# Performance work log

Hardware: AMD Instinct MI355X
Metric: run time of the kernel (lower is better)

Reference implementation:

```python
import jax, jax.numpy as jnp
import numpy as np

N, E = 50000, 800000
DIN, DH, DOUT = 128, 128, 64


def setup_inputs() -> dict:
    key = jax.random.key(0)
    ks = jax.random.split(key, 18)
    s = 0.05
    inp = {
        "x": jax.random.normal(ks[0], (N, DIN), dtype=jnp.float32),
        "edge_index": jax.random.randint(ks[1], (2, E), 0, N, dtype=jnp.int64),
        # conv1 MLP: Linear(DIN,DH), Linear(DH,DH)
        "c1_w1": jax.random.normal(ks[2], (DIN, DH), dtype=jnp.float32) * s,
        "c1_b1": jax.random.normal(ks[3], (DH,), dtype=jnp.float32) * s,
        "c1_w2": jax.random.normal(ks[4], (DH, DH), dtype=jnp.float32) * s,
        "c1_b2": jax.random.normal(ks[5], (DH,), dtype=jnp.float32) * s,
        # conv2 MLP
        "c2_w1": jax.random.normal(ks[6], (DH, DH), dtype=jnp.float32) * s,
        "c2_b1": jax.random.normal(ks[7], (DH,), dtype=jnp.float32) * s,
        "c2_w2": jax.random.normal(ks[8], (DH, DH), dtype=jnp.float32) * s,
        "c2_b2": jax.random.normal(ks[9], (DH,), dtype=jnp.float32) * s,
        # conv3 MLP
        "c3_w1": jax.random.normal(ks[10], (DH, DH), dtype=jnp.float32) * s,
        "c3_b1": jax.random.normal(ks[11], (DH,), dtype=jnp.float32) * s,
        "c3_w2": jax.random.normal(ks[12], (DH, DH), dtype=jnp.float32) * s,
        "c3_b2": jax.random.normal(ks[13], (DH,), dtype=jnp.float32) * s,
        # output head
        "lin1_w": jax.random.normal(ks[14], (DH, DH), dtype=jnp.float32) * s,
        "lin1_b": jax.random.normal(ks[15], (DH,), dtype=jnp.float32) * s,
        "lin2_w": jax.random.normal(ks[16], (DH, DOUT), dtype=jnp.float32) * s,
        "lin2_b": jax.random.normal(ks[17], (DOUT,), dtype=jnp.float32) * s,
    }
    return inp


def _gin_conv(h, src, dst, w1, b1, w2, b2):
    # PyG GINConv, eps=0: MLP((1+eps)*x + sum_{j->i} x_j)
    agg = jax.ops.segment_sum(h[src], dst, num_segments=h.shape[0])  # [N, D]
    z = h + agg
    z = jax.nn.relu(z @ w1 + b1)
    return jax.nn.relu(z @ w2 + b2)


def reference(x, edge_index, c1_w1, c1_b1, c1_w2, c1_b2,
              c2_w1, c2_b1, c2_w2, c2_b2,
              c3_w1, c3_b1, c3_w2, c3_b2,
              lin1_w, lin1_b, lin2_w, lin2_b):
    src, dst = edge_index[0], edge_index[1]
    h = _gin_conv(x, src, dst, c1_w1, c1_b1, c1_w2, c1_b2)
    h = jax.nn.relu(h)  # redundant after MLP ReLU, but faithful to source
    h = _gin_conv(h, src, dst, c2_w1, c2_b1, c2_w2, c2_b2)
    h = jax.nn.relu(h)
    h = _gin_conv(h, src, dst, c3_w1, c3_b1, c3_w2, c3_b2)
    h = jax.nn.relu(h @ lin1_w + lin1_b)
    return h @ lin2_w + lin2_b  # [N, DOUT]
```

## Files before the change

kernel.cpp:

```cpp
#include <hip/hip_runtime.h>
#include <hip/hip_bf16.h>

typedef __attribute__((ext_vector_type(8))) short bf16x8;
typedef __attribute__((ext_vector_type(4))) float f32x4;

#define DH 128
#define DOUT 64

static __device__ __forceinline__ unsigned short f2bf(float f) {
    __hip_bfloat16 h = __float2bfloat16(f);
    return *(unsigned short*)&h;
}
static __device__ __forceinline__ void acc2(float& a0, float& a1, unsigned int u) {
    a0 += __uint_as_float(u << 16);
    a1 += __uint_as_float(u & 0xffff0000u);
}


struct WPrep {
    const float* src[8];
    unsigned short* dst[8];
};

__global__ void prep_kernel(const float* __restrict__ x, unsigned short* __restrict__ xb,
                            unsigned short* __restrict__ hA, unsigned short* __restrict__ hB,
                            int n4, WPrep p, int* __restrict__ cnt,
                            int* __restrict__ esrc, int Epad, int N_) {
    int id = blockIdx.x * blockDim.x + threadIdx.x;
    if (id < n4) {
        float4 v = ((const float4*)x)[id];
        ushort4 b;
        b.x = f2bf(v.x); b.y = f2bf(v.y); b.z = f2bf(v.z); b.w = f2bf(v.w);
        ((ushort4*)xb)[id] = b;
        return;
    }
    id -= n4;
    if (id < N_) { cnt[id] = 0; return; }
    id -= N_;
    if (id < 7 * 16384 + 8192) {
        int m, off;
        if (id < 7 * 16384) { m = id >> 14; off = id & 16383; }
        else { m = 7; off = id - 7 * 16384; }
        int shift = (m == 7) ? 6 : 7;
        int nc = 1 << shift;
        int k = off >> shift;
        int n = off & (nc - 1);
        p.dst[m][n * 128 + k] = f2bf(p.src[m][off]);
        return;
    }
    id -= 7 * 16384 + 8192;
    if (id < 3 * 128) {
        int j = id & 127, w = id >> 7;
        if (w == 0) xb[(size_t)N_ * 128 + j] = 0;
        else if (w == 1) hA[(size_t)N_ * 128 + j] = 0;
        else hB[(size_t)N_ * 128 + j] = 0;
        return;
    }
    id -= 384;
    if (id < Epad) esrc[id] = N_ << 8;
}


__global__ void hist_kernel(const int* __restrict__ dst, int* __restrict__ cnt,
                            int* __restrict__ rank, int E, int n) {
    int e = blockIdx.x * blockDim.x + threadIdx.x;
    if (e < E) {
        int d = dst[e];
        if ((unsigned)d < (unsigned)n) rank[e] = atomicAdd(&cnt[d], 1);
    }
}

__global__ void scan1_kernel(const int* __restrict__ cnt, int* __restrict__ rp_part,
                             int* __restrict__ bsum, int n) {
    __shared__ int s[256];
    int tid = threadIdx.x;
    int i = blockIdx.x * 256 + tid;
    int v = (i < n) ? ((cnt[i] + 7) & ~7) : 0;
    s[tid] = v;
    __syncthreads();
    for (int off = 1; off < 256; off <<= 1) {
        int t = (tid >= off) ? s[tid - off] : 0;
        __syncthreads();
        s[tid] += t;
        __syncthreads();
    }
    if (i <= n) rp_part[i] = s[tid] - v;
    if (tid == 255) bsum[blockIdx.x] = s[255];
}

__global__ void scan2_kernel(int* __restrict__ bsum, int nb) {
    __shared__ int s[256];
    int tid = threadIdx.x;
    int v = (tid < nb) ? bsum[tid] : 0;
    s[tid] = v;
    __syncthreads();
    for (int off = 1; off < 256; off <<= 1) {
        int t = (tid >= off) ? s[tid - off] : 0;
        __syncthreads();
        s[tid] += t;
        __syncthreads();
    }
    if (tid < nb) bsum[tid] = s[tid] - v;
}

__global__ void scan3_fill_kernel(const int* __restrict__ rp_part, const int* __restrict__ bsum,
                                  int* __restrict__ row_ptr,
                                  const int* __restrict__ src, const int* __restrict__ dst,
                                  const int* __restrict__ rank, int* __restrict__ esrc,
                                  int n, int E) {
    int gid = blockIdx.x * blockDim.x + threadIdx.x;
    if (gid <= n) row_ptr[gid] = rp_part[gid] + bsum[gid >> 8];
    if (gid < E) {
        int d = dst[gid];
        if ((unsigned)d < (unsigned)n)
            esrc[rp_part[d] + bsum[d >> 8] + rank[gid]] = src[gid] << 8;
    }
}


template <bool HEAD>
__launch_bounds__(256, 8)
__global__ void layer_kernel(const unsigned short* __restrict__ h,
                             const int* __restrict__ rp,
                             const int* __restrict__ esrc,
                             const unsigned short* __restrict__ W1t,
                             const float* __restrict__ b1,
                             const unsigned short* __restrict__ W2t,
                             const float* __restrict__ b2,
                             const unsigned short* __restrict__ W3t,
                             const float* __restrict__ b3,
                             const unsigned short* __restrict__ W4t,
                             const float* __restrict__ b4,
                             void* __restrict__ outp, int M) {
    constexpr int LDA = 128 + 8;
    __shared__ __align__(16) unsigned short As[16][LDA];
    __shared__ __align__(16) unsigned short Zs[16][LDA];

    int tid = threadIdx.x;
    int wave = __builtin_amdgcn_readfirstlane(tid >> 6);
    int lane = tid & 63;
    int row0 = blockIdx.x * 16;
    int nd0 = row0 + wave * 4;

    const char* hc = (const char*)h;
    unsigned voff = (unsigned)lane << 2;

#pragma unroll
    for (int i = 0; i < 4; ++i) {
        int nd = nd0 + i;
        int rb = __builtin_amdgcn_readfirstlane(rp[nd]);
        int re = __builtin_amdgcn_readfirstlane(rp[nd + 1]);
        unsigned su = *(const unsigned*)(hc + ((size_t)(unsigned)nd << 8) + voff);
        float a0 = 0.f, a1 = 0.f;
        for (int r = rb; r < re; r += 8) {
            int o0 = __builtin_amdgcn_readfirstlane(esrc[r + 0]);
            int o1 = __builtin_amdgcn_readfirstlane(esrc[r + 1]);
            int o2 = __builtin_amdgcn_readfirstlane(esrc[r + 2]);
            int o3 = __builtin_amdgcn_readfirstlane(esrc[r + 3]);
            int o4 = __builtin_amdgcn_readfirstlane(esrc[r + 4]);
            int o5 = __builtin_amdgcn_readfirstlane(esrc[r + 5]);
            int o6 = __builtin_amdgcn_readfirstlane(esrc[r + 6]);
            int o7 = __builtin_amdgcn_readfirstlane(esrc[r + 7]);
            unsigned u0 = *(const unsigned*)(hc + o0 + voff);
            unsigned u1 = *(const unsigned*)(hc + o1 + voff);
            unsigned u2 = *(const unsigned*)(hc + o2 + voff);
            unsigned u3 = *(const unsigned*)(hc + o3 + voff);
            unsigned u4 = *(const unsigned*)(hc + o4 + voff);
            unsigned u5 = *(const unsigned*)(hc + o5 + voff);
            unsigned u6 = *(const unsigned*)(hc + o6 + voff);
            unsigned u7 = *(const unsigned*)(hc + o7 + voff);
            acc2(a0, a1, u0);
            acc2(a0, a1, u1);
            acc2(a0, a1, u2);
            acc2(a0, a1, u3);
            acc2(a0, a1, u4);
            acc2(a0, a1, u5);
            acc2(a0, a1, u6);
            acc2(a0, a1, u7);
        }
        acc2(a0, a1, su);
        unsigned pv = (unsigned)f2bf(a0) | ((unsigned)f2bf(a1) << 16);
        *(unsigned*)&As[wave * 4 + i][lane * 2] = pv;
    }
    __syncthreads();

    int quad = lane >> 4;
    int l16 = lane & 15;

    bf16x8 af[4];
#pragma unroll
    for (int kt = 0; kt < 4; ++kt)
        af[kt] = *(const bf16x8*)(&As[l16][kt * 32 + quad * 8]);
#pragma unroll
    for (int p = 0; p < 2; ++p) {
        int ncol = (wave * 2 + p) * 16 + l16;
        const unsigned short* wp = W1t + ncol * 128 + quad * 8;
        f32x4 a = {0.f, 0.f, 0.f, 0.f};
#pragma unroll
        for (int kt = 0; kt < 4; ++kt)
            a = __builtin_amdgcn_mfma_f32_16x16x32_bf16(
                af[kt], *(const bf16x8*)(wp + kt * 32), a, 0, 0, 0);
        float bs = b1[ncol];
#pragma unroll
        for (int r = 0; r < 4; ++r) {
            float v = a[r] + bs;
            if (v < 0.f) v = 0.f;
            Zs[quad * 4 + r][ncol] = f2bf(v);
        }
    }
    __syncthreads();

    bf16x8 zf[4];
#pragma unroll
    for (int kt = 0; kt < 4; ++kt)
        zf[kt] = *(const bf16x8*)(&Zs[l16][kt * 32 + quad * 8]);
#pragma unroll
    for (int p = 0; p < 2; ++p) {
        int ncol = (wave * 2 + p) * 16 + l16;
        const unsigned short* wp = W2t + ncol * 128 + quad * 8;
        f32x4 a = {0.f, 0.f, 0.f, 0.f};
#pragma unroll
        for (int kt = 0; kt < 4; ++kt)
            a = __builtin_amdgcn_mfma_f32_16x16x32_bf16(
                zf[kt], *(const bf16x8*)(wp + kt * 32), a, 0, 0, 0);
        float bs = b2[ncol];
#pragma unroll
        for (int r = 0; r < 4; ++r) {
            float v = a[r] + bs;
            if (v < 0.f) v = 0.f;
            if (HEAD) {
                As[quad * 4 + r][ncol] = f2bf(v);
            } else {
                int grow = row0 + quad * 4 + r;
                if (grow < M)
                    ((unsigned short*)outp)[(size_t)grow * 128 + ncol] = f2bf(v);
            }
        }
    }

    if (HEAD) {
        __syncthreads();
        bf16x8 hf[4];
#pragma unroll
        for (int kt = 0; kt < 4; ++kt)
            hf[kt] = *(const bf16x8*)(&As[l16][kt * 32 + quad * 8]);
#pragma unroll
        for (int p = 0; p < 2; ++p) {
            int ncol = (wave * 2 + p) * 16 + l16;
            const unsigned short* wp = W3t + ncol * 128 + quad * 8;
            f32x4 a = {0.f, 0.f, 0.f, 0.f};
#pragma unroll
            for (int kt = 0; kt < 4; ++kt)
                a = __builtin_amdgcn_mfma_f32_16x16x32_bf16(
                    hf[kt], *(const bf16x8*)(wp + kt * 32), a, 0, 0, 0);
            float bs = b3[ncol];
#pragma unroll
            for (int r = 0; r < 4; ++r) {
                float v = a[r] + bs;
                if (v < 0.f) v = 0.f;
                Zs[quad * 4 + r][ncol] = f2bf(v);
            }
        }
        __syncthreads();
        bf16x8 gf[4];
#pragma unroll
        for (int kt = 0; kt < 4; ++kt)
            gf[kt] = *(const bf16x8*)(&Zs[l16][kt * 32 + quad * 8]);
        {
            int ncol = wave * 16 + l16;
            const unsigned short* wp = W4t + ncol * 128 + quad * 8;
            f32x4 a = {0.f, 0.f, 0.f, 0.f};
#pragma unroll
            for (int kt = 0; kt < 4; ++kt)
                a = __builtin_amdgcn_mfma_f32_16x16x32_bf16(
                    gf[kt], *(const bf16x8*)(wp + kt * 32), a, 0, 0, 0);
            float bs = b4[ncol];
#pragma unroll
            for (int r = 0; r < 4; ++r) {
                int grow = row0 + quad * 4 + r;
                if (grow < M)
                    ((float*)outp)[(size_t)grow * 64 + ncol] = a[r] + bs;
            }
        }
    }
}


extern "C" void kernel_launch(void* const* d_in, const int* in_sizes, int n_in,
                              void* d_out, int out_size, void* d_ws, size_t ws_size,
                              hipStream_t stream) {
    const float* x = (const float*)d_in[0];
    const int* ei = (const int*)d_in[1];
    int N = in_sizes[0] / DH;
    int E = in_sizes[1] / 2;
    const int* src = ei;
    const int* dstv = ei + E;
    int Epad = E + 7 * N + 1024;

    char* ws = (char*)d_ws;
    size_t off = 0;
    auto alloc = [&](size_t bytes) -> void* {
        void* p = ws + off;
        off += (bytes + 255) & ~(size_t)255;
        return p;
    };
    unsigned short* xb = (unsigned short*)alloc((size_t)(N + 1) * DH * 2);
    unsigned short* hA = (unsigned short*)alloc((size_t)(N + 1) * DH * 2);
    unsigned short* hB = (unsigned short*)alloc((size_t)(N + 1) * DH * 2);
    unsigned short* wt[8];
    for (int m = 0; m < 8; ++m) wt[m] = (unsigned short*)alloc(16384 * 2);
    int* cnt     = (int*)alloc((size_t)N * 4);
    int* rp_part = (int*)alloc((size_t)(N + 1) * 4);
    int* row_ptr = (int*)alloc((size_t)(N + 1) * 4);
    int* rank    = (int*)alloc((size_t)E * 4);
    int* bsum    = (int*)alloc(256 * 4);
    int* esrc    = (int*)alloc((size_t)Epad * 4);

    WPrep wp;
    wp.src[0] = (const float*)d_in[2];
    wp.src[1] = (const float*)d_in[4];
    wp.src[2] = (const float*)d_in[6];
    wp.src[3] = (const float*)d_in[8];
    wp.src[4] = (const float*)d_in[10];
    wp.src[5] = (const float*)d_in[12];
    wp.src[6] = (const float*)d_in[14];
    wp.src[7] = (const float*)d_in[16];
    for (int m = 0; m < 8; ++m) wp.dst[m] = wt[m];
    int n4 = N * DH / 4;
    int prep_items = n4 + N + 7 * 16384 + 8192 + 384 + Epad;
    prep_kernel<<<(prep_items + 255) / 256, 256, 0, stream>>>(
        x, xb, hA, hB, n4, wp, cnt, esrc, Epad, N);

    int nb = (N + 1 + 255) / 256;
    int eb = (E + 255) / 256;
    hist_kernel<<<eb, 256, 0, stream>>>(dstv, cnt, rank, E, N);
    scan1_kernel<<<nb, 256, 0, stream>>>(cnt, rp_part, bsum, N);
    scan2_kernel<<<1, 256, 0, stream>>>(bsum, nb);
    scan3_fill_kernel<<<eb, 256, 0, stream>>>(rp_part, bsum, row_ptr,
                                              src, dstv, rank, esrc, N, E);

    int gb = (N + 15) / 16;

    const float* c1b1 = (const float*)d_in[3];
    const float* c1b2 = (const float*)d_in[5];
    const float* c2b1 = (const float*)d_in[7];
    const float* c2b2 = (const float*)d_in[9];
    const float* c3b1 = (const float*)d_in[11];
    const float* c3b2 = (const float*)d_in[13];
    const float* l1b  = (const float*)d_in[15];
    const float* l2b  = (const float*)d_in[17];

    layer_kernel<false><<<gb, 256, 0, stream>>>(
        xb, row_ptr, esrc, wt[0], c1b1, wt[1], c1b2,
        nullptr, nullptr, nullptr, nullptr, hA, N);
    layer_kernel<false><<<gb, 256, 0, stream>>>(
        hA, row_ptr, esrc, wt[2], c2b1, wt[3], c2b2,
        nullptr, nullptr, nullptr, nullptr, hB, N);
    layer_kernel<true><<<gb, 256, 0, stream>>>(
        hB, row_ptr, esrc, wt[4], c3b1, wt[5], c3b2,
        wt[6], l1b, wt[7], l2b, d_out, N);
}
```

Baseline: 323.7 us.

## Stage block edge indices in LDS and software-pipeline the neighbor gather

```diff
diff --git a/kernel.cpp b/kernel.cpp
--- a/kernel.cpp
+++ b/kernel.cpp
@@ -119,7 +119,7 @@
 
 
 template <bool HEAD>
-__launch_bounds__(256, 8)
+__launch_bounds__(256, 6)
 __global__ void layer_kernel(const unsigned short* __restrict__ h,
                              const int* __restrict__ rp,
                              const int* __restrict__ esrc,
@@ -133,8 +133,10 @@
                              const float* __restrict__ b4,
                              void* __restrict__ outp, int M) {
     constexpr int LDA = 128 + 8;
+    constexpr int CAP = 2048;
     __shared__ __align__(16) unsigned short As[16][LDA];
     __shared__ __align__(16) unsigned short Zs[16][LDA];
+    __shared__ int sIdx[CAP];
 
     int tid = threadIdx.x;
     int wave = __builtin_amdgcn_readfirstlane(tid >> 6);
@@ -145,41 +147,62 @@
     const char* hc = (const char*)h;
     unsigned voff = (unsigned)lane << 2;
 
+    int wb = rp[row0];
+    int C = rp[min(row0 + 16, M)] - wb;
+
+    int b[4], e[4];
+    unsigned su[4];
+    float a0[4] = {0.f, 0.f, 0.f, 0.f}, a1[4] = {0.f, 0.f, 0.f, 0.f};
 #pragma unroll
     for (int i = 0; i < 4; ++i) {
         int nd = nd0 + i;
-        int rb = __builtin_amdgcn_readfirstlane(rp[nd]);
-        int re = __builtin_amdgcn_readfirstlane(rp[nd + 1]);
-        unsigned su = *(const unsigned*)(hc + ((size_t)(unsigned)nd << 8) + voff);
-        float a0 = 0.f, a1 = 0.f;
-        for (int r = rb; r < re; r += 8) {
-            int o0 = __builtin_amdgcn_readfirstlane(esrc[r + 0]);
-            int o1 = __builtin_amdgcn_readfirstlane(esrc[r + 1]);
-            int o2 = __builtin_amdgcn_readfirstlane(esrc[r + 2]);
-            int o3 = __builtin_amdgcn_readfirstlane(esrc[r + 3]);
-            int o4 = __builtin_amdgcn_readfirstlane(esrc[r + 4]);
-            int o5 = __builtin_amdgcn_readfirstlane(esrc[r + 5]);
-            int o6 = __builtin_amdgcn_readfirstlane(esrc[r + 6]);
-            int o7 = __builtin_amdgcn_readfirstlane(esrc[r + 7]);
-            unsigned u0 = *(const unsigned*)(hc + o0 + voff);
-            unsigned u1 = *(const unsigned*)(hc + o1 + voff);
-            unsigned u2 = *(const unsigned*)(hc + o2 + voff);
-            unsigned u3 = *(const unsigned*)(hc + o3 + voff);
-            unsigned u4 = *(const unsigned*)(hc + o4 + voff);
-            unsigned u5 = *(const unsigned*)(hc + o5 + voff);
-            unsigned u6 = *(const unsigned*)(hc + o6 + voff);
-            unsigned u7 = *(const unsigned*)(hc + o7 + voff);
-            acc2(a0, a1, u0);
-            acc2(a0, a1, u1);
-            acc2(a0, a1, u2);
-            acc2(a0, a1, u3);
-            acc2(a0, a1, u4);
-            acc2(a0, a1, u5);
-            acc2(a0, a1, u6);
-            acc2(a0, a1, u7);
-        }
-        acc2(a0, a1, su);
-        unsigned pv = (unsigned)f2bf(a0) | ((unsigned)f2bf(a1) << 16);
+        int ndc = min(nd, M);
+        int nd1 = min(nd + 1, M);
+        b[i] = rp[ndc] - wb;
+        e[i] = rp[nd1] - wb;
+        su[i] = *(const unsigned*)(hc + ((size_t)(unsigned)ndc << 8) + voff);
+    }
+
+    for (int p0 = 0; p0 < C; p0 += CAP) {
+        int cend = min(C, p0 + CAP);
+        for (int i = tid; i < cend - p0; i += 256) sIdx[i] = esrc[wb + p0 + i];
+        __syncthreads();
+#pragma unroll
+        for (int i = 0; i < 4; ++i) {
+            int nb = max(b[i], p0) - p0;
+            int ne = min(e[i], cend) - p0;
+            if (nb < ne) {
+                int idxA[8];
+                unsigned uA[8];
+#pragma unroll
+                for (int t = 0; t < 8; ++t) idxA[t] = sIdx[nb + t];
+#pragma unroll
+                for (int t = 0; t < 8; ++t)
+                    uA[t] = *(const unsigned*)(hc + (unsigned)idxA[t] + voff);
+                for (int r = nb + 8; r < ne; r += 8) {
+                    int idxB[8];
+                    unsigned uB[8];
+#pragma unroll
+                    for (int t = 0; t < 8; ++t) idxB[t] = sIdx[r + t];
+#pragma unroll
+                    for (int t = 0; t < 8; ++t)
+                        uB[t] = *(const unsigned*)(hc + (unsigned)idxB[t] + voff);
+#pragma unroll
+                    for (int t = 0; t < 8; ++t) acc2(a0[i], a1[i], uA[t]);
+#pragma unroll
+                    for (int t = 0; t < 8; ++t) { uA[t] = uB[t]; }
+                }
+#pragma unroll
+                for (int t = 0; t < 8; ++t) acc2(a0[i], a1[i], uA[t]);
+            }
+        }
+        __syncthreads();
+    }
+
+#pragma unroll
+    for (int i = 0; i < 4; ++i) {
+        acc2(a0[i], a1[i], su[i]);
+        unsigned pv = (unsigned)f2bf(a0[i]) | ((unsigned)f2bf(a1[i]) << 16);
         *(unsigned*)&As[wave * 4 + i][lane * 2] = pv;
     }
     __syncthreads();
```

Result: no change. 321.5 us (-0.7%).

## Drop CSR padding to multiples of 8 and fuse preprocessing launches

Applied to the files above, without the earlier changes.

```diff
diff --git a/kernel.cpp b/kernel.cpp
--- a/kernel.cpp
+++ b/kernel.cpp
@@ -22,10 +22,11 @@
     unsigned short* dst[8];
 };
 
-__global__ void prep_kernel(const float* __restrict__ x, unsigned short* __restrict__ xb,
-                            unsigned short* __restrict__ hA, unsigned short* __restrict__ hB,
-                            int n4, WPrep p, int* __restrict__ cnt,
-                            int* __restrict__ esrc, int Epad, int N_) {
+__global__ void prep_hist_kernel(const float* __restrict__ x, unsigned short* __restrict__ xb,
+                                 unsigned short* __restrict__ hA, unsigned short* __restrict__ hB,
+                                 int n4, WPrep p,
+                                 const int* __restrict__ dstv, int* __restrict__ cnt,
+                                 int* __restrict__ rank, int E, int N_) {
     int id = blockIdx.x * blockDim.x + threadIdx.x;
     if (id < n4) {
         float4 v = ((const float4*)x)[id];
@@ -35,8 +36,6 @@
         return;
     }
     id -= n4;
-    if (id < N_) { cnt[id] = 0; return; }
-    id -= N_;
     if (id < 7 * 16384 + 8192) {
         int m, off;
         if (id < 7 * 16384) { m = id >> 14; off = id & 16383; }
@@ -57,25 +56,19 @@
         return;
     }
     id -= 384;
-    if (id < Epad) esrc[id] = N_ << 8;
-}
-
-
-__global__ void hist_kernel(const int* __restrict__ dst, int* __restrict__ cnt,
-                            int* __restrict__ rank, int E, int n) {
-    int e = blockIdx.x * blockDim.x + threadIdx.x;
-    if (e < E) {
-        int d = dst[e];
-        if ((unsigned)d < (unsigned)n) rank[e] = atomicAdd(&cnt[d], 1);
-    }
-}
+    if (id < E) {
+        int d = dstv[id];
+        if ((unsigned)d < (unsigned)N_) rank[id] = atomicAdd(&cnt[d], 1);
+    }
+}
+
 
 __global__ void scan1_kernel(const int* __restrict__ cnt, int* __restrict__ rp_part,
                              int* __restrict__ bsum, int n) {
     __shared__ int s[256];
     int tid = threadIdx.x;
     int i = blockIdx.x * 256 + tid;
-    int v = (i < n) ? ((cnt[i] + 7) & ~7) : 0;
+    int v = (i < n) ? cnt[i] : 0;
     s[tid] = v;
     __syncthreads();
     for (int off = 1; off < 256; off <<= 1) {
@@ -88,32 +81,34 @@
     if (tid == 255) bsum[blockIdx.x] = s[255];
 }
 
-__global__ void scan2_kernel(int* __restrict__ bsum, int nb) {
-    __shared__ int s[256];
-    int tid = threadIdx.x;
-    int v = (tid < nb) ? bsum[tid] : 0;
-    s[tid] = v;
-    __syncthreads();
-    for (int off = 1; off < 256; off <<= 1) {
-        int t = (tid >= off) ? s[tid - off] : 0;
-        __syncthreads();
-        s[tid] += t;
-        __syncthreads();
-    }
-    if (tid < nb) bsum[tid] = s[tid] - v;
-}
-
 __global__ void scan3_fill_kernel(const int* __restrict__ rp_part, const int* __restrict__ bsum,
                                   int* __restrict__ row_ptr,
                                   const int* __restrict__ src, const int* __restrict__ dst,
                                   const int* __restrict__ rank, int* __restrict__ esrc,
-                                  int n, int E) {
-    int gid = blockIdx.x * blockDim.x + threadIdx.x;
-    if (gid <= n) row_ptr[gid] = rp_part[gid] + bsum[gid >> 8];
+                                  int n, int E, int nb) {
+    __shared__ int sb[256];
+    int tid = threadIdx.x;
+    {
+        int v = (tid < nb) ? bsum[tid] : 0;
+        sb[tid] = v;
+        __syncthreads();
+        for (int off = 1; off < 256; off <<= 1) {
+            int t = (tid >= off) ? sb[tid - off] : 0;
+            __syncthreads();
+            sb[tid] += t;
+            __syncthreads();
+        }
+        int incl = sb[tid];
+        __syncthreads();
+        sb[tid] = incl - v;
+        __syncthreads();
+    }
+    int gid = blockIdx.x * 256 + tid;
+    if (gid <= n) row_ptr[gid] = rp_part[gid] + sb[gid >> 8];
     if (gid < E) {
         int d = dst[gid];
         if ((unsigned)d < (unsigned)n)
-            esrc[rp_part[d] + bsum[d >> 8] + rank[gid]] = src[gid] << 8;
+            esrc[rp_part[d] + sb[d >> 8] + rank[gid]] = src[gid] << 8;
     }
 }
 
@@ -147,28 +142,28 @@
 
 #pragma unroll
     for (int i = 0; i < 4; ++i) {
-        int nd = nd0 + i;
-        int rb = __builtin_amdgcn_readfirstlane(rp[nd]);
-        int re = __builtin_amdgcn_readfirstlane(rp[nd + 1]);
+        int nd = min(nd0 + i, M - 1);
+        int rb = rp[nd], re = rp[nd + 1];
         unsigned su = *(const unsigned*)(hc + ((size_t)(unsigned)nd << 8) + voff);
         float a0 = 0.f, a1 = 0.f;
-        for (int r = rb; r < re; r += 8) {
-            int o0 = __builtin_amdgcn_readfirstlane(esrc[r + 0]);
-            int o1 = __builtin_amdgcn_readfirstlane(esrc[r + 1]);
-            int o2 = __builtin_amdgcn_readfirstlane(esrc[r + 2]);
-            int o3 = __builtin_amdgcn_readfirstlane(esrc[r + 3]);
-            int o4 = __builtin_amdgcn_readfirstlane(esrc[r + 4]);
-            int o5 = __builtin_amdgcn_readfirstlane(esrc[r + 5]);
-            int o6 = __builtin_amdgcn_readfirstlane(esrc[r + 6]);
-            int o7 = __builtin_amdgcn_readfirstlane(esrc[r + 7]);
-            unsigned u0 = *(const unsigned*)(hc + o0 + voff);
-            unsigned u1 = *(const unsigned*)(hc + o1 + voff);
-            unsigned u2 = *(const unsigned*)(hc + o2 + voff);
-            unsigned u3 = *(const unsigned*)(hc + o3 + voff);
-            unsigned u4 = *(const unsigned*)(hc + o4 + voff);
-            unsigned u5 = *(const unsigned*)(hc + o5 + voff);
-            unsigned u6 = *(const unsigned*)(hc + o6 + voff);
-            unsigned u7 = *(const unsigned*)(hc + o7 + voff);
+        int j = rb;
+        for (; j + 8 <= re; j += 8) {
+            int o0 = esrc[j + 0];
+            int o1 = esrc[j + 1];
+            int o2 = esrc[j + 2];
+            int o3 = esrc[j + 3];
+            int o4 = esrc[j + 4];
+            int o5 = esrc[j + 5];
+            int o6 = esrc[j + 6];
+            int o7 = esrc[j + 7];
+            unsigned u0 = *(const unsigned*)(hc + (unsigned)o0 + voff);
+            unsigned u1 = *(const unsigned*)(hc + (unsigned)o1 + voff);
+            unsigned u2 = *(const unsigned*)(hc + (unsigned)o2 + voff);
+            unsigned u3 = *(const unsigned*)(hc + (unsigned)o3 + voff);
+            unsigned u4 = *(const unsigned*)(hc + (unsigned)o4 + voff);
+            unsigned u5 = *(const unsigned*)(hc + (unsigned)o5 + voff);
+            unsigned u6 = *(const unsigned*)(hc + (unsigned)o6 + voff);
+            unsigned u7 = *(const unsigned*)(hc + (unsigned)o7 + voff);
             acc2(a0, a1, u0);
             acc2(a0, a1, u1);
             acc2(a0, a1, u2);
@@ -177,6 +172,18 @@
             acc2(a0, a1, u5);
             acc2(a0, a1, u6);
             acc2(a0, a1, u7);
+        }
+        for (; j + 2 <= re; j += 2) {
+            int o0 = esrc[j], o1 = esrc[j + 1];
+            unsigned u0 = *(const unsigned*)(hc + (unsigned)o0 + voff);
+            unsigned u1 = *(const unsigned*)(hc + (unsigned)o1 + voff);
+            acc2(a0, a1, u0);
+            acc2(a0, a1, u1);
+        }
+        for (; j < re; ++j) {
+            int o0 = esrc[j];
+            unsigned u0 = *(const unsigned*)(hc + (unsigned)o0 + voff);
+            acc2(a0, a1, u0);
         }
         acc2(a0, a1, su);
         unsigned pv = (unsigned)f2bf(a0) | ((unsigned)f2bf(a1) << 16);
@@ -295,7 +302,6 @@
     int E = in_sizes[1] / 2;
     const int* src = ei;
     const int* dstv = ei + E;
-    int Epad = E + 7 * N + 1024;
 
     char* ws = (char*)d_ws;
     size_t off = 0;
@@ -314,7 +320,7 @@
     int* row_ptr = (int*)alloc((size_t)(N + 1) * 4);
     int* rank    = (int*)alloc((size_t)E * 4);
     int* bsum    = (int*)alloc(256 * 4);
-    int* esrc    = (int*)alloc((size_t)Epad * 4);
+    int* esrc    = (int*)alloc((size_t)E * 4);
 
     WPrep wp;
     wp.src[0] = (const float*)d_in[2];
@@ -326,18 +332,21 @@
     wp.src[6] = (const float*)d_in[14];
     wp.src[7] = (const float*)d_in[16];
     for (int m = 0; m < 8; ++m) wp.dst[m] = wt[m];
+
+    hipMemsetAsync(cnt, 0, (size_t)N * 4, stream);
+
     int n4 = N * DH / 4;
-    int prep_items = n4 + N + 7 * 16384 + 8192 + 384 + Epad;
-    prep_kernel<<<(prep_items + 255) / 256, 256, 0, stream>>>(
-        x, xb, hA, hB, n4, wp, cnt, esrc, Epad, N);
-
-    int nb = (N + 1 + 255) / 256;
+    int prep_items = n4 + 7 * 16384 + 8192 + 384 + E;
+    prep_hist_kernel<<<(prep_items + 255) / 256, 256, 0, stream>>>(
+        x, xb, hA, hB, n4, wp, dstv, cnt, rank, E, N);
+
+    int nb = (N + 255) / 256;
+    int nb1 = (N + 1 + 255) / 256;
     int eb = (E + 255) / 256;
-    hist_kernel<<<eb, 256, 0, stream>>>(dstv, cnt, rank, E, N);
-    scan1_kernel<<<nb, 256, 0, stream>>>(cnt, rp_part, bsum, N);
-    scan2_kernel<<<1, 256, 0, stream>>>(bsum, nb);
-    scan3_fill_kernel<<<eb, 256, 0, stream>>>(rp_part, bsum, row_ptr,
-                                              src, dstv, rank, esrc, N, E);
+    scan1_kernel<<<nb1, 256, 0, stream>>>(cnt, rp_part, bsum, N);
+    int s3blocks = eb > nb1 ? eb : nb1;
+    scan3_fill_kernel<<<s3blocks, 256, 0, stream>>>(rp_part, bsum, row_ptr,
+                                                    src, dstv, rank, esrc, N, E, nb);
 
     int gb = (N + 15) / 16;
 
```

Result: slower. 331.2 us (+2.3%).
